# Optimization experiments

Measured on AMD Instinct MI355X. Metric: run time of the kernel, lower is better.

## Reference

```python
import jax, jax.numpy as jnp
import numpy as np

N_NODES = 50000
N_EDGES = 800000
IN_NF = 128
OUT_NF = 128
HID = 128
EDGE_NF = 16
N_LAYERS = 4
EPS = 1e-5


def _ln(x, g, b):
    mu = jnp.mean(x, axis=-1, keepdims=True)
    var = jnp.mean(jnp.square(x - mu), axis=-1, keepdims=True)
    return (x - mu) * jax.lax.rsqrt(var + EPS) * g + b


def setup_inputs() -> dict:
    key = jax.random.key(0)
    ks = iter(jax.random.split(key, 64))

    def lin(out_d, in_d):
        w = jax.random.normal(next(ks), (out_d, in_d), dtype=jnp.float32) * 0.02
        b = jnp.zeros((out_d,), dtype=jnp.float32)
        return w, b

    def stack(fn):
        outs = [fn() for _ in range(N_LAYERS)]
        return tuple(jnp.stack([o[i] for o in outs]) for i in range(len(outs[0])))

    h = jax.random.normal(next(ks), (N_NODES, IN_NF), dtype=jnp.float32)
    edges = jax.random.randint(next(ks), (2, N_EDGES), 0, N_NODES, dtype=jnp.int32)
    edge_attr = jax.random.normal(next(ks), (N_EDGES, EDGE_NF), dtype=jnp.float32)

    emb_in_w1, emb_in_b1 = lin(HID, IN_NF)
    emb_in_w2, emb_in_b2 = lin(HID, HID)
    emb_out_w1, emb_out_b1 = lin(HID, HID)
    emb_out_w2, emb_out_b2 = lin(OUT_NF, HID)

    norm_g, norm_b = stack(lambda: (jnp.ones((HID,), jnp.float32), jnp.zeros((HID,), jnp.float32)))
    edge_w1, edge_b1 = stack(lambda: lin(HID, 2 * HID + EDGE_NF))
    edge_ln_g, edge_ln_b = stack(lambda: (jnp.ones((HID,), jnp.float32), jnp.zeros((HID,), jnp.float32)))
    edge_w2, edge_b2 = stack(lambda: lin(HID, HID))
    node_w1, node_b1 = stack(lambda: lin(HID, 2 * HID))
    node_ln_g, node_ln_b = stack(lambda: (jnp.ones((HID,), jnp.float32), jnp.zeros((HID,), jnp.float32)))
    node_w2, node_b2 = stack(lambda: lin(HID, HID))

    return dict(h=h, edges=edges, edge_attr=edge_attr,
                emb_in_w1=emb_in_w1, emb_in_b1=emb_in_b1, emb_in_w2=emb_in_w2, emb_in_b2=emb_in_b2,
                norm_g=norm_g, norm_b=norm_b,
                edge_w1=edge_w1, edge_b1=edge_b1, edge_ln_g=edge_ln_g, edge_ln_b=edge_ln_b,
                edge_w2=edge_w2, edge_b2=edge_b2,
                node_w1=node_w1, node_b1=node_b1, node_ln_g=node_ln_g, node_ln_b=node_ln_b,
                node_w2=node_w2, node_b2=node_b2,
                emb_out_w1=emb_out_w1, emb_out_b1=emb_out_b1, emb_out_w2=emb_out_w2, emb_out_b2=emb_out_b2)


def _gnn(h, edges, edge_attr,
         emb_in_w1, emb_in_b1, emb_in_w2, emb_in_b2,
         norm_g, norm_b, edge_w1, edge_b1, edge_ln_g, edge_ln_b, edge_w2, edge_b2,
         node_w1, node_b1, node_ln_g, node_ln_b, node_w2, node_b2,
         emb_out_w1, emb_out_b1, emb_out_w2, emb_out_b2):
    row, col = edges[0], edges[1]
    n = h.shape[0]

    # embedding_in: Linear -> SiLU -> Linear
    h = jax.nn.silu(h @ emb_in_w1.T + emb_in_b1) @ emb_in_w2.T + emb_in_b2

    def layer(h, p):
        (ng, nb, ew1, eb1, elg, elb, ew2, eb2, nw1, nb1, nlg, nlb, nw2, nb2) = p
        hn = _ln(h, ng, nb)                                   # pre-layer LayerNorm
        # message: gather -> Linear -> LN -> SiLU -> Linear
        eh = jnp.concatenate([hn[row], hn[col], edge_attr], axis=1)  # [E, 2H+Ef]
        m = jax.nn.silu(_ln(eh @ ew1.T + eb1, elg, elb)) @ ew2.T + eb2  # [E, H]
        # aggregate: scatter-add over source nodes
        agg = jax.ops.segment_sum(m, row, num_segments=n)     # [N, H]
        cat = jnp.concatenate([hn, agg], axis=1)              # [N, 2H]
        dh = jax.nn.silu(_ln(cat @ nw1.T + nb1, nlg, nlb)) @ nw2.T + nb2
        return hn + dh, None

    params = (norm_g, norm_b, edge_w1, edge_b1, edge_ln_g, edge_ln_b, edge_w2, edge_b2,
              node_w1, node_b1, node_ln_g, node_ln_b, node_w2, node_b2)
    h, _ = jax.lax.scan(layer, h, params)

    # embedding_out
    return jax.nn.silu(h @ emb_out_w1.T + emb_out_b1) @ emb_out_w2.T + emb_out_b2


def reference(h, edges, edge_attr,
              emb_in_w1, emb_in_b1, emb_in_w2, emb_in_b2,
              norm_g, norm_b, edge_w1, edge_b1, edge_ln_g, edge_ln_b, edge_w2, edge_b2,
              node_w1, node_b1, node_ln_g, node_ln_b, node_w2, node_b2,
              emb_out_w1, emb_out_b1, emb_out_w2, emb_out_b2):
    return _gnn(h, edges, edge_attr,
                emb_in_w1, emb_in_b1, emb_in_w2, emb_in_b2,
                norm_g, norm_b, edge_w1, edge_b1, edge_ln_g, edge_ln_b, edge_w2, edge_b2,
                node_w1, node_b1, node_ln_g, node_ln_b, node_w2, node_b2,
                emb_out_w1, emb_out_b1, emb_out_w2, emb_out_b2)
```

## Files before the change

kernel.cpp:

```cpp
#include <hip/hip_runtime.h>
#include <math.h>

#define NN 50000
#define NE 800000
#define HID 128
#define NNH ((size_t)NN * HID)
#define NPAD 50176

typedef __attribute__((ext_vector_type(8))) short short8;
typedef __attribute__((ext_vector_type(4))) float f32x4;

__device__ __forceinline__ ushort f2bf(float f) {
  unsigned u = __float_as_uint(f);
  unsigned r = (u + 0x7fffu + ((u >> 16) & 1u)) >> 16;
  return (ushort)r;
}
__device__ __forceinline__ float bf2f(ushort h) {
  return __uint_as_float(((unsigned)h) << 16);
}
__device__ __forceinline__ float silu_f(float x) { return x / (1.0f + __expf(-x)); }

__global__ __launch_bounds__(256) void zero_i(int* __restrict__ p, int n)
{
  int i = blockIdx.x * 256 + threadIdx.x;
  if (i < n) p[i] = 0;
}

__global__ __launch_bounds__(256) void count_src(const int* __restrict__ src, int* __restrict__ cnt)
{
  int e = blockIdx.x * 256 + threadIdx.x;
  if (e < NE) atomicAdd(&cnt[src[e]], 1);
}

__global__ __launch_bounds__(1024) void scan_excl(const int* __restrict__ cnt, int* __restrict__ base, int n)
{
  __shared__ int ws[16];
  int t = threadIdx.x;
  const int per = (n + 1023) / 1024;
  int s0 = t * per;
  int sum = 0;
  for (int i = 0; i < per; ++i) { int idx = s0 + i; if (idx < n) sum += cnt[idx]; }
  int lane = t & 63, w = t >> 6;
  int v = sum;
  #pragma unroll
  for (int m = 1; m < 64; m <<= 1) { int o = __shfl_up(v, m, 64); if (lane >= m) v += o; }
  if (lane == 63) ws[w] = v;
  __syncthreads();
  if (t == 0) { int a = 0; for (int i = 0; i < 16; ++i) { int x = ws[i]; ws[i] = a; a += x; } }
  __syncthreads();
  int run = ws[w] + v - sum;
  for (int i = 0; i < per; ++i) {
    int idx = s0 + i;
    if (idx < n) { base[idx] = run; run += cnt[idx]; }
  }
}

__global__ __launch_bounds__(256) void place_edges(const int* __restrict__ src, const int* __restrict__ dst,
    const int* __restrict__ base, int* __restrict__ cur,
    int* __restrict__ dst_s, int* __restrict__ perm)
{
  int e = blockIdx.x * 256 + threadIdx.x;
  if (e >= NE) return;
  int s = src[e];
  int p = base[s] + atomicAdd(&cur[s], 1);
  dst_s[p] = dst[e]; perm[p] = e;
}

__global__ __launch_bounds__(256) void permute_ea_bf(const float4* __restrict__ ea,
    const int* __restrict__ perm, ushort* __restrict__ ea_s)
{
  int i = blockIdx.x * 256 + threadIdx.x;
  if (i >= NE * 4) return;
  int e = i >> 2, q = i & 3;
  float4 v = ea[(size_t)perm[e] * 4 + q];
  uint2 p;
  p.x = (uint)f2bf(v.x) | ((uint)f2bf(v.y) << 16);
  p.y = (uint)f2bf(v.z) | ((uint)f2bf(v.w) << 16);
  *(uint2*)&ea_s[(size_t)e * 16 + q * 4] = p;
}

__global__ __launch_bounds__(256) void cvt4(const float* __restrict__ s0, const float* __restrict__ s1,
    const float* __restrict__ s2, const float* __restrict__ s3, ushort* __restrict__ d)
{
  int i = blockIdx.x * 256 + threadIdx.x;
  if (i >= 65536) return;
  const float* s = (i < 16384) ? s0 : (i < 32768) ? s1 : (i < 49152) ? s2 : s3;
  d[i] = f2bf(s[i & 16383]);
}
__global__ __launch_bounds__(256) void cvt_wab(const float* __restrict__ s, ushort* __restrict__ d)
{
  int i = blockIdx.x * 256 + threadIdx.x;
  if (i >= 131072) return;
  int l = i >> 15, rem = i & 32767;
  int r = rem >> 7, c = rem & 127;
  int srow = r & 127, scol = ((r >> 7) << 7) + c;
  d[l * 104448 + r * 128 + c] = f2bf(s[(size_t)l * 34816 + srow * 272 + scol]);
}
__global__ __launch_bounds__(256) void cvt_std(const float* __restrict__ s, ushort* __restrict__ d,
    int rows, int cols, int lss)
{
  int i = blockIdx.x * 256 + threadIdx.x;
  int n = 4 * rows * cols;
  if (i >= n) return;
  int rc = rows * cols;
  int l = i / rc, rem = i - l * rc;
  d[l * 104448 + rem] = f2bf(s[(size_t)l * lss + rem]);
}

__global__ __launch_bounds__(128) void fold_w(const float* __restrict__ nw1,
    const float* __restrict__ ew2, const float* __restrict__ eb2,
    ushort* __restrict__ wu_base, float* __restrict__ nv)
{
  __shared__ float red[2];
  int bid = blockIdx.x;
  int l = bid >> 7, m = bid & 127;
  int j = threadIdx.x;
  const float* n1row = nw1 + (size_t)l * 32768 + (size_t)m * 256;
  const float* n1b = n1row + 128;
  const float* w2 = ew2 + (size_t)l * 16384;
  float s = 0.f;
  for (int k = 0; k < 128; ++k) s = fmaf(n1b[k], w2[k * 128 + j], s);
  ushort* lb = wu_base + (size_t)l * 104448;
  lb[32768 + m * 128 + j] = f2bf(s);
  lb[49152 + m * 128 + j] = f2bf(n1row[j]);
  float p = n1b[j] * eb2[l * 128 + j];
  #pragma unroll
  for (int mm = 1; mm < 64; mm <<= 1) p += __shfl_xor(p, mm, 64);
  if ((j & 63) == 0) red[j >> 6] = p;
  __syncthreads();
  if (j == 0) nv[l * 128 + m] = red[0] + red[1];
}

__global__ __launch_bounds__(256) void emb2(
    const float* __restrict__ A,
    const ushort* __restrict__ W1, const float* __restrict__ b1,
    const ushort* __restrict__ W2, const float* __restrict__ b2,
    float* __restrict__ C, int n)
{
  __shared__ ushort Al[64][136];
  const int tid = threadIdx.x;
  const int n0 = blockIdx.x * 64;

  #pragma unroll
  for (int i = 0; i < 8; ++i) {
    int s = tid + i * 256;
    int row = s >> 5, c4 = (s & 31) * 4;
    int gr = n0 + row;
    float4 v = make_float4(0.f, 0.f, 0.f, 0.f);
    if (gr < n) v = *(const float4*)(A + (size_t)gr * HID + c4);
    uint2 p;
    p.x = (uint)f2bf(v.x) | ((uint)f2bf(v.y) << 16);
    p.y = (uint)f2bf(v.z) | ((uint)f2bf(v.w) << 16);
    *(uint2*)&Al[row][c4] = p;
  }
  __syncthreads();

  const int w = tid >> 6, l = tid & 63;
  const int lr = l & 15, lh = l >> 4;

  f32x4 zf = {0.f, 0.f, 0.f, 0.f};
  f32x4 acc[8];
  #pragma unroll
  for (int nt = 0; nt < 8; ++nt) acc[nt] = zf;

  #pragma unroll
  for (int q = 0; q < 4; ++q) {
    short8 af = *(const short8*)&Al[w * 16 + lr][q * 32 + lh * 8];
    #pragma unroll
    for (int nt = 0; nt < 8; ++nt) {
      short8 bf = *(const short8*)(W1 + (size_t)(nt * 16 + lr) * HID + q * 32 + lh * 8);
      acc[nt] = __builtin_amdgcn_mfma_f32_16x16x32_bf16(af, bf, acc[nt], 0, 0, 0);
    }
  }

  float vb[8];
  #pragma unroll
  for (int nt = 0; nt < 8; ++nt) vb[nt] = b1[nt * 16 + lr];

  #pragma unroll
  for (int r = 0; r < 4; ++r) {
    int row = w * 16 + lh * 4 + r;
    #pragma unroll
    for (int nt = 0; nt < 8; ++nt)
      Al[row][nt * 16 + lr] = f2bf(silu_f(acc[nt][r] + vb[nt]));
  }

  f32x4 acc2[8];
  #pragma unroll
  for (int nt = 0; nt < 8; ++nt) acc2[nt] = zf;
  #pragma unroll
  for (int q = 0; q < 4; ++q) {
    short8 af = *(const short8*)&Al[w * 16 + lr][q * 32 + lh * 8];
    #pragma unroll
    for (int nt = 0; nt < 8; ++nt) {
      short8 bf = *(const short8*)(W2 + (size_t)(nt * 16 + lr) * HID + q * 32 + lh * 8);
      acc2[nt] = __builtin_amdgcn_mfma_f32_16x16x32_bf16(af, bf, acc2[nt], 0, 0, 0);
    }
  }

  float vb2[8];
  #pragma unroll
  for (int nt = 0; nt < 8; ++nt) vb2[nt] = b2[nt * 16 + lr];
  #pragma unroll
  for (int r = 0; r < 4; ++r) {
    int row = n0 + w * 16 + lh * 4 + r;
    if (row < n) {
      float* cr = C + (size_t)row * HID;
      #pragma unroll
      for (int nt = 0; nt < 8; ++nt)
        cr[nt * 16 + lr] = acc2[nt][r] + vb2[nt];
    }
  }
}

__global__ __launch_bounds__(256) void pab_ln(
    const float* __restrict__ Hraw, const ushort* __restrict__ Wab,
    const float* __restrict__ lg, const float* __restrict__ lbp,
    const float* __restrict__ eb1,
    float* __restrict__ Hn, float* __restrict__ Pa, float* __restrict__ Pb, int n)
{
  __shared__ float Hs[64][132];
  __shared__ ushort Al[64][136];
  const int tid = threadIdx.x;
  const int n0 = blockIdx.x * 64;

  #pragma unroll
  for (int i = 0; i < 8; ++i) {
    int s = tid + i * 256;
    int row = s >> 5, c4 = (s & 31) * 4;
    int gr = n0 + row;
    float4 v = make_float4(0.f, 0.f, 0.f, 0.f);
    if (gr < n) v = *(const float4*)(Hraw + (size_t)gr * HID + c4);
    *(float4*)&Hs[row][c4] = v;
  }
  __syncthreads();

  const int w = tid >> 6, l = tid & 63;
  const int lr = l & 15, lh = l >> 4;

  {
    const int row = w * 16 + lr;
    float s1 = 0.f, s2 = 0.f;
    #pragma unroll
    for (int j = 0; j < 8; ++j) {
      float4 v = *(float4*)&Hs[row][lh * 32 + j * 4];
      s1 += v.x + v.y + v.z + v.w;
      s2 += v.x * v.x + v.y * v.y + v.z * v.z + v.w * v.w;
    }
    s1 += __shfl_xor(s1, 16, 64); s1 += __shfl_xor(s1, 32, 64);
    s2 += __shfl_xor(s2, 16, 64); s2 += __shfl_xor(s2, 32, 64);
    float mu = s1 * (1.0f / 128.0f);
    float var = s2 * (1.0f / 128.0f) - mu * mu;
    float rs = rsqrtf(var + 1e-5f);
    int gr = n0 + row;
    #pragma unroll
    for (int j = 0; j < 8; ++j) {
      int c = lh * 32 + j * 4;
      float4 v = *(float4*)&Hs[row][c];
      float4 o;
      o.x = (v.x - mu) * rs * lg[c + 0] + lbp[c + 0];
      o.y = (v.y - mu) * rs * lg[c + 1] + lbp[c + 1];
      o.z = (v.z - mu) * rs * lg[c + 2] + lbp[c + 2];
      o.w = (v.w - mu) * rs * lg[c + 3] + lbp[c + 3];
      if (gr < n) *(float4*)(Hn + (size_t)gr * HID + c) = o;
      uint2 p;
      p.x = (uint)f2bf(o.x) | ((uint)f2bf(o.y) << 16);
      p.y = (uint)f2bf(o.z) | ((uint)f2bf(o.w) << 16);
      *(uint2*)&Al[row][c] = p;
    }
  }
  __syncthreads();

  f32x4 zf = {0.f, 0.f, 0.f, 0.f};
  f32x4 acc[16];
  #pragma unroll
  for (int nt = 0; nt < 16; ++nt) acc[nt] = zf;

  #pragma unroll
  for (int q = 0; q < 4; ++q) {
    short8 af = *(const short8*)&Al[w * 16 + lr][q * 32 + lh * 8];
    #pragma unroll
    for (int nt = 0; nt < 16; ++nt) {
      short8 bf = *(const short8*)(Wab + (size_t)(nt * 16 + lr) * HID + q * 32 + lh * 8);
      acc[nt] = __builtin_amdgcn_mfma_f32_16x16x32_bf16(af, bf, acc[nt], 0, 0, 0);
    }
  }

  float be[8];
  #pragma unroll
  for (int nt = 0; nt < 8; ++nt) be[nt] = eb1[nt * 16 + lr];

  #pragma unroll
  for (int r = 0; r < 4; ++r) {
    int row = n0 + w * 16 + lh * 4 + r;
    if (row >= n) break;
    float* pa = Pa + (size_t)row * HID;
    float* pb = Pb + (size_t)row * HID;
    #pragma unroll
    for (int nt = 0; nt < 8; ++nt) {
      int col = nt * 16 + lr;
      pa[col] = acc[nt][r] + be[nt];
      pb[col] = acc[nt + 8][r];
    }
  }
}

__global__ __launch_bounds__(256) void node_edge(
    const float* __restrict__ Pa, const float* __restrict__ Pb,
    const ushort* __restrict__ ea_bf,
    const int* __restrict__ dst_s,
    const int* __restrict__ ebase, const int* __restrict__ deg,
    const float* __restrict__ w1c,
    const float* __restrict__ elg, const float* __restrict__ elb,
    float* __restrict__ S, int n)
{
  const int tid = threadIdx.x;
  const int wv = __builtin_amdgcn_readfirstlane(tid >> 6);
  const int lane = tid & 63;
  const int node = blockIdx.x * 4 + wv;
  if (node >= n) return;
  const int c0 = lane * 2;

  float w10[16], w11[16];
  {
    const float* wr0 = w1c + (size_t)c0 * 272 + 256;
    const float* wr1 = wr0 + 272;
    #pragma unroll
    for (int q = 0; q < 4; ++q) {
      float4 a = *(const float4*)(wr0 + q * 4);
      float4 b = *(const float4*)(wr1 + q * 4);
      w10[q * 4 + 0] = a.x; w10[q * 4 + 1] = a.y; w10[q * 4 + 2] = a.z; w10[q * 4 + 3] = a.w;
      w11[q * 4 + 0] = b.x; w11[q * 4 + 1] = b.y; w11[q * 4 + 2] = b.z; w11[q * 4 + 3] = b.w;
    }
  }
  const float g0 = elg[c0], g1 = elg[c0 + 1];
  const float b0 = elb[c0], b1 = elb[c0 + 1];
  const float pax = Pa[(size_t)node * HID + c0];
  const float pay = Pa[(size_t)node * HID + c0 + 1];

  const int beg = __builtin_amdgcn_readfirstlane(ebase[node]);
  const int dg  = __builtin_amdgcn_readfirstlane(deg[node]);

  float a0 = 0.f, a1 = 0.f;

  uint4 eA0 = make_uint4(0,0,0,0), eB0 = eA0, eA1 = eA0, eB1 = eA0;
  float2 p0 = make_float2(0.f, 0.f), p1 = p0;

  auto LOADE = [&](int idx, uint4& ea, uint4& eb, float2& pb) {
    int eu = __builtin_amdgcn_readfirstlane(beg + idx);
    int d  = dst_s[eu];
    ea = *(const uint4*)(ea_bf + (size_t)eu * 16);
    eb = *(const uint4*)(ea_bf + (size_t)eu * 16 + 8);
    pb = *(const float2*)(Pb + (size_t)d * HID + c0);
  };
  auto PROCESS = [&](const uint4& eaA, const uint4& eaB, const float2& pbc) {
    float ev[16];
    uint u;
    u = eaA.x; ev[0]  = __uint_as_float(u << 16); ev[1]  = __uint_as_float(u & 0xffff0000u);
    u = eaA.y; ev[2]  = __uint_as_float(u << 16); ev[3]  = __uint_as_float(u & 0xffff0000u);
    u = eaA.z; ev[4]  = __uint_as_float(u << 16); ev[5]  = __uint_as_float(u & 0xffff0000u);
    u = eaA.w; ev[6]  = __uint_as_float(u << 16); ev[7]  = __uint_as_float(u & 0xffff0000u);
    u = eaB.x; ev[8]  = __uint_as_float(u << 16); ev[9]  = __uint_as_float(u & 0xffff0000u);
    u = eaB.y; ev[10] = __uint_as_float(u << 16); ev[11] = __uint_as_float(u & 0xffff0000u);
    u = eaB.z; ev[12] = __uint_as_float(u << 16); ev[13] = __uint_as_float(u & 0xffff0000u);
    u = eaB.w; ev[14] = __uint_as_float(u << 16); ev[15] = __uint_as_float(u & 0xffff0000u);

    float x0 = pax + pbc.x;
    float x1 = pay + pbc.y;
    #pragma unroll
    for (int k = 0; k < 16; ++k) {
      x0 = fmaf(ev[k], w10[k], x0);
      x1 = fmaf(ev[k], w11[k], x1);
    }
    float s1 = x0 + x1, s2 = x0 * x0 + x1 * x1;
    #pragma unroll
    for (int m = 1; m < 64; m <<= 1) {
      s1 += __shfl_xor(s1, m, 64);
      s2 += __shfl_xor(s2, m, 64);
    }
    float mu = s1 * (1.0f / 128.0f);
    float var = s2 * (1.0f / 128.0f) - mu * mu;
    float rs = rsqrtf(var + 1e-5f);
    a0 += silu_f((x0 - mu) * rs * g0 + b0);
    a1 += silu_f((x1 - mu) * rs * g1 + b1);
  };

  if (dg > 0) LOADE(0, eA0, eB0, p0);
  if (dg > 1) LOADE(1, eA1, eB1, p1);

  for (int i = 0; i < dg; i += 2) {
    uint4 nA0 = make_uint4(0,0,0,0), nB0 = nA0, nA1 = nA0, nB1 = nA0;
    float2 np0 = make_float2(0.f, 0.f), np1 = np0;
    if (i + 2 < dg) LOADE(i + 2, nA0, nB0, np0);
    if (i + 3 < dg) LOADE(i + 3, nA1, nB1, np1);

    PROCESS(eA0, eB0, p0);
    if (i + 1 < dg) PROCESS(eA1, eB1, p1);

    eA0 = nA0; eB0 = nB0; p0 = np0;
    eA1 = nA1; eB1 = nB1; p1 = np1;
  }

  *(float2*)(S + (size_t)node * HID + c0) = make_float2(a0, a1);
}

__global__ __launch_bounds__(256) void node_mlp(
    const float* __restrict__ Hn, const float* __restrict__ S,
    const ushort* __restrict__ N1a, const ushort* __restrict__ W2N, const ushort* __restrict__ N2,
    const float* __restrict__ nb1, const float* __restrict__ nv, const int* __restrict__ deg,
    const float* __restrict__ lng, const float* __restrict__ lnb, const float* __restrict__ nb2,
    float* __restrict__ C, int n)
{
  __shared__ ushort Ahn[64][136];
  __shared__ ushort Ah[64][136];
  __shared__ ushort Alo[64][136];
  const int tid = threadIdx.x;
  const int n0 = blockIdx.x * 64;

  #pragma unroll
  for (int i = 0; i < 8; ++i) {
    int s = tid + i * 256;
    int row = s >> 5, c4 = (s & 31) * 4;
    int gr = n0 + row;
    float4 vh = make_float4(0.f, 0.f, 0.f, 0.f);
    float4 vs = make_float4(0.f, 0.f, 0.f, 0.f);
    if (gr < n) {
      vh = *(const float4*)(Hn + (size_t)gr * HID + c4);
      vs = *(const float4*)(S + (size_t)gr * HID + c4);
    }
    uint2 ph;
    ph.x = (uint)f2bf(vh.x) | ((uint)f2bf(vh.y) << 16);
    ph.y = (uint)f2bf(vh.z) | ((uint)f2bf(vh.w) << 16);
    *(uint2*)&Ahn[row][c4] = ph;
    ushort hx = f2bf(vs.x), hy = f2bf(vs.y), hz = f2bf(vs.z), hw = f2bf(vs.w);
    uint2 ps, pl;
    ps.x = (uint)hx | ((uint)hy << 16);
    ps.y = (uint)hz | ((uint)hw << 16);
    pl.x = (uint)f2bf(vs.x - bf2f(hx)) | ((uint)f2bf(vs.y - bf2f(hy)) << 16);
    pl.y = (uint)f2bf(vs.z - bf2f(hz)) | ((uint)f2bf(vs.w - bf2f(hw)) << 16);
    *(uint2*)&Ah[row][c4]  = ps;
    *(uint2*)&Alo[row][c4] = pl;
  }
  __syncthreads();

  const int w = tid >> 6, l = tid & 63;
  const int lr = l & 15, lh = l >> 4;

  f32x4 zf = {0.f, 0.f, 0.f, 0.f};
  f32x4 acc[8];
  #pragma unroll
  for (int nt = 0; nt < 8; ++nt) acc[nt] = zf;

  #pragma unroll
  for (int q = 0; q < 4; ++q) {
    short8 an = *(const short8*)&Ahn[w * 16 + lr][q * 32 + lh * 8];
    short8 ah = *(const short8*)&Ah[w * 16 + lr][q * 32 + lh * 8];
    short8 al = *(const short8*)&Alo[w * 16 + lr][q * 32 + lh * 8];
    #pragma unroll
    for (int nt = 0; nt < 8; ++nt) {
      short8 b1f = *(const short8*)(N1a + (size_t)(nt * 16 + lr) * HID + q * 32 + lh * 8);
      short8 b2f = *(const short8*)(W2N + (size_t)(nt * 16 + lr) * HID + q * 32 + lh * 8);
      acc[nt] = __builtin_amdgcn_mfma_f32_16x16x32_bf16(an, b1f, acc[nt], 0, 0, 0);
      acc[nt] = __builtin_amdgcn_mfma_f32_16x16x32_bf16(ah, b2f, acc[nt], 0, 0, 0);
      acc[nt] = __builtin_amdgcn_mfma_f32_16x16x32_bf16(al, b2f, acc[nt], 0, 0, 0);
    }
  }

  float vb[8], vn[8], gv[8], bv[8];
  #pragma unroll
  for (int nt = 0; nt < 8; ++nt) {
    int col = nt * 16 + lr;
    vb[nt] = nb1[col]; vn[nt] = nv[col];
    gv[nt] = lng[col]; bv[nt] = lnb[col];
  }

  #pragma unroll
  for (int r = 0; r < 4; ++r) {
    int row = n0 + w * 16 + lh * 4 + r;
    float degf = (row < n) ? (float)deg[row] : 0.f;
    float vals[8];
    #pragma unroll
    for (int nt = 0; nt < 8; ++nt) vals[nt] = acc[nt][r] + vb[nt] + degf * vn[nt];
    float s1 = 0.f, s2 = 0.f;
    #pragma unroll
    for (int nt = 0; nt < 8; ++nt) { s1 += vals[nt]; s2 += vals[nt] * vals[nt]; }
    #pragma unroll
    for (int m = 1; m < 16; m <<= 1) { s1 += __shfl_xor(s1, m, 64); s2 += __shfl_xor(s2, m, 64); }
    float mu = s1 * (1.0f / 128.0f);
    float var = s2 * (1.0f / 128.0f) - mu * mu;
    float rs = rsqrtf(var + 1e-5f);
    int lrow = w * 16 + lh * 4 + r;
    #pragma unroll
    for (int nt = 0; nt < 8; ++nt)
      Ahn[lrow][nt * 16 + lr] = f2bf(silu_f((vals[nt] - mu) * rs * gv[nt] + bv[nt]));
  }

  f32x4 acc2[8];
  #pragma unroll
  for (int nt = 0; nt < 8; ++nt) acc2[nt] = zf;
  #pragma unroll
  for (int q = 0; q < 4; ++q) {
    short8 af = *(const short8*)&Ahn[w * 16 + lr][q * 32 + lh * 8];
    #pragma unroll
    for (int nt = 0; nt < 8; ++nt) {
      short8 bf = *(const short8*)(N2 + (size_t)(nt * 16 + lr) * HID + q * 32 + lh * 8);
      acc2[nt] = __builtin_amdgcn_mfma_f32_16x16x32_bf16(af, bf, acc2[nt], 0, 0, 0);
    }
  }

  float vb2[8];
  #pragma unroll
  for (int nt = 0; nt < 8; ++nt) vb2[nt] = nb2[nt * 16 + lr];
  #pragma unroll
  for (int r = 0; r < 4; ++r) {
    int row = n0 + w * 16 + lh * 4 + r;
    if (row < n) {
      const float* hr = Hn + (size_t)row * HID;
      float* cr = C + (size_t)row * HID;
      #pragma unroll
      for (int nt = 0; nt < 8; ++nt) {
        int col = nt * 16 + lr;
        cr[col] = hr[col] + acc2[nt][r] + vb2[nt];
      }
    }
  }
}

extern "C" void kernel_launch(void* const* d_in, const int* in_sizes, int n_in,
                              void* d_out, int out_size, void* d_ws, size_t ws_size,
                              hipStream_t stream)
{
  const float* in_h  = (const float*)d_in[0];
  const int*   edges = (const int*)d_in[1];
  const float* ea    = (const float*)d_in[2];
  const float* ei_w1 = (const float*)d_in[3];
  const float* ei_b1 = (const float*)d_in[4];
  const float* ei_w2 = (const float*)d_in[5];
  const float* ei_b2 = (const float*)d_in[6];
  const float* ng    = (const float*)d_in[7];
  const float* nbp   = (const float*)d_in[8];
  const float* ew1   = (const float*)d_in[9];
  const float* eb1   = (const float*)d_in[10];
  const float* elg   = (const float*)d_in[11];
  const float* elb   = (const float*)d_in[12];
  const float* ew2   = (const float*)d_in[13];
  const float* eb2   = (const float*)d_in[14];
  const float* nw1   = (const float*)d_in[15];
  const float* nb1   = (const float*)d_in[16];
  const float* nlg   = (const float*)d_in[17];
  const float* nlb   = (const float*)d_in[18];
  const float* nw2   = (const float*)d_in[19];
  const float* nb2   = (const float*)d_in[20];
  const float* eo_w1 = (const float*)d_in[21];
  const float* eo_b1 = (const float*)d_in[22];
  const float* eo_w2 = (const float*)d_in[23];
  const float* eo_b2 = (const float*)d_in[24];

  float* wf    = (float*)d_ws;
  float* B_h   = wf;
  float* B_hn  = wf + NNH;
  float* B_S   = wf + 2 * NNH;
  float* B_tmp = wf + 3 * NNH;
  float* B_pb  = wf + 4 * NNH;

  const size_t WOFF = 5 * NNH;
  ushort* wu = (ushort*)(wf + WOFF);
  const size_t SOFF = WOFF + 262144;
  int* dst_s = (int*)(wf + SOFF);
  int* cnt   = dst_s + NE;
  int* cur   = cnt + NPAD;
  int* base  = cur + NPAD;
  ushort* ea_s = (ushort*)(base + NPAD);
  float* nvb = (float*)(ea_s + (size_t)NE * 16);
  int* perm  = (int*)B_S;

  const int NB  = (NN + 63) / 64;
  const int NBE = (NN + 3) / 4;
  const int NEB = (NE + 255) / 256;

  const int* erow = edges;
  const int* ecol = edges + NE;

  zero_i<<<(2 * NPAD + 255) / 256, 256, 0, stream>>>(cnt, 2 * NPAD);
  count_src<<<NEB, 256, 0, stream>>>(erow, cnt);
  scan_excl<<<1, 1024, 0, stream>>>(cnt, base, NN);
  place_edges<<<NEB, 256, 0, stream>>>(erow, ecol, base, cur, dst_s, perm);
  permute_ea_bf<<<(NE * 4 + 255) / 256, 256, 0, stream>>>((const float4*)ea, perm, ea_s);

  cvt4<<<256, 256, 0, stream>>>(ei_w1, ei_w2, eo_w1, eo_w2, wu);
  cvt_wab<<<512, 256, 0, stream>>>(ew1, wu + 65536);
  cvt_std<<<(4 * 16384 + 255) / 256, 256, 0, stream>>>(nw2, wu + 65536 + 81920, 128, 128, 16384);
  fold_w<<<512, 128, 0, stream>>>(nw1, ew2, eb2, wu + 65536, nvb);

  emb2<<<NB, 256, 0, stream>>>(in_h, wu, ei_b1, wu + 16384, ei_b2, B_h, NN);

  for (int lyr = 0; lyr < 4; ++lyr) {
    ushort* lb = wu + 65536 + lyr * 104448;
    pab_ln<<<NB, 256, 0, stream>>>(B_h, lb, ng + 128 * lyr, nbp + 128 * lyr,
        eb1 + 128 * lyr, B_hn, B_tmp, B_pb, NN);
    node_edge<<<NBE, 256, 0, stream>>>(B_tmp, B_pb, ea_s, dst_s, base, cnt,
        ew1 + 34816 * lyr, elg + 128 * lyr, elb + 128 * lyr, B_S, NN);
    node_mlp<<<NB, 256, 0, stream>>>(B_hn, B_S, lb + 49152, lb + 32768, lb + 81920,
        nb1 + 128 * lyr, nvb + 128 * lyr, cnt,
        nlg + 128 * lyr, nlb + 128 * lyr, nb2 + 128 * lyr, B_h, NN);
  }

  emb2<<<NB, 256, 0, stream>>>(B_h, wu + 32768, eo_b1, wu + 49152, eo_b2, (float*)d_out, NN);
}
```

Before: 1.424 ms.

## Process two edges per wave with half-wave split and fp16 dot2 edge projection

Restructures the per-node edge kernel so each half-wave (32 lanes, 4 channels each) handles a different edge at once, which halves the LayerNorm shuffle-reduction depth and combines the two halves at the end. Edge attributes are now stored as fp16 instead of bf16, so the 16-wide edge-attribute projection can use packed fdot2 instructions against fp16 copies of the weights. It also adds an early exit for nodes with no edges. The costs are reduced precision in the edge-weight dot products, wasted lanes on odd-degree tails, and more live registers per lane.

```diff
diff --git a/kernel.cpp b/kernel.cpp
--- a/kernel.cpp
+++ b/kernel.cpp
@@ -9,6 +9,7 @@
 
 typedef __attribute__((ext_vector_type(8))) short short8;
 typedef __attribute__((ext_vector_type(4))) float f32x4;
+typedef __attribute__((ext_vector_type(2))) _Float16 half2v;
 
 __device__ __forceinline__ ushort f2bf(float f) {
   unsigned u = __float_as_uint(f);
@@ -17,6 +18,17 @@
 }
 __device__ __forceinline__ float bf2f(ushort h) {
   return __uint_as_float(((unsigned)h) << 16);
+}
+__device__ __forceinline__ ushort f2h_bits(float f) {
+  _Float16 h = (_Float16)f;
+  ushort u;
+  __builtin_memcpy(&u, &h, 2);
+  return u;
+}
+__device__ __forceinline__ half2v u2h(uint u) {
+  half2v h;
+  __builtin_memcpy(&h, &u, 4);
+  return h;
 }
 __device__ __forceinline__ float silu_f(float x) { return x / (1.0f + __expf(-x)); }
 
@@ -66,7 +78,7 @@
   dst_s[p] = dst[e]; perm[p] = e;
 }
 
-__global__ __launch_bounds__(256) void permute_ea_bf(const float4* __restrict__ ea,
+__global__ __launch_bounds__(256) void permute_ea_h(const float4* __restrict__ ea,
     const int* __restrict__ perm, ushort* __restrict__ ea_s)
 {
   int i = blockIdx.x * 256 + threadIdx.x;
@@ -74,8 +86,8 @@
   int e = i >> 2, q = i & 3;
   float4 v = ea[(size_t)perm[e] * 4 + q];
   uint2 p;
-  p.x = (uint)f2bf(v.x) | ((uint)f2bf(v.y) << 16);
-  p.y = (uint)f2bf(v.z) | ((uint)f2bf(v.w) << 16);
+  p.x = (uint)f2h_bits(v.x) | ((uint)f2h_bits(v.y) << 16);
+  p.y = (uint)f2h_bits(v.z) | ((uint)f2h_bits(v.w) << 16);
   *(uint2*)&ea_s[(size_t)e * 16 + q * 4] = p;
 }
 
@@ -307,7 +319,7 @@
 
 __global__ __launch_bounds__(256) void node_edge(
     const float* __restrict__ Pa, const float* __restrict__ Pb,
-    const ushort* __restrict__ ea_bf,
+    const ushort* __restrict__ ea_h,
     const int* __restrict__ dst_s,
     const int* __restrict__ ebase, const int* __restrict__ deg,
     const float* __restrict__ w1c,
@@ -319,89 +331,102 @@
   const int lane = tid & 63;
   const int node = blockIdx.x * 4 + wv;
   if (node >= n) return;
-  const int c0 = lane * 2;
-
-  float w10[16], w11[16];
-  {
-    const float* wr0 = w1c + (size_t)c0 * 272 + 256;
-    const float* wr1 = wr0 + 272;
-    #pragma unroll
-    for (int q = 0; q < 4; ++q) {
-      float4 a = *(const float4*)(wr0 + q * 4);
-      float4 b = *(const float4*)(wr1 + q * 4);
-      w10[q * 4 + 0] = a.x; w10[q * 4 + 1] = a.y; w10[q * 4 + 2] = a.z; w10[q * 4 + 3] = a.w;
-      w11[q * 4 + 0] = b.x; w11[q * 4 + 1] = b.y; w11[q * 4 + 2] = b.z; w11[q * 4 + 3] = b.w;
-    }
-  }
-  const float g0 = elg[c0], g1 = elg[c0 + 1];
-  const float b0 = elb[c0], b1 = elb[c0 + 1];
-  const float pax = Pa[(size_t)node * HID + c0];
-  const float pay = Pa[(size_t)node * HID + c0 + 1];
+  const int half = lane >> 5;
+  const int l32 = lane & 31;
+  const int c0 = l32 * 4;
 
   const int beg = __builtin_amdgcn_readfirstlane(ebase[node]);
   const int dg  = __builtin_amdgcn_readfirstlane(deg[node]);
 
-  float a0 = 0.f, a1 = 0.f;
-
-  uint4 eA0 = make_uint4(0,0,0,0), eB0 = eA0, eA1 = eA0, eB1 = eA0;
-  float2 p0 = make_float2(0.f, 0.f), p1 = p0;
-
-  auto LOADE = [&](int idx, uint4& ea, uint4& eb, float2& pb) {
-    int eu = __builtin_amdgcn_readfirstlane(beg + idx);
-    int d  = dst_s[eu];
-    ea = *(const uint4*)(ea_bf + (size_t)eu * 16);
-    eb = *(const uint4*)(ea_bf + (size_t)eu * 16 + 8);
-    pb = *(const float2*)(Pb + (size_t)d * HID + c0);
+  if (dg == 0) {
+    if (half == 0)
+      *(float4*)(S + (size_t)node * HID + c0) = make_float4(0.f, 0.f, 0.f, 0.f);
+    return;
+  }
+
+  half2v w1h[4][8];
+  #pragma unroll
+  for (int c = 0; c < 4; ++c) {
+    const float* wr = w1c + (size_t)(c0 + c) * 272 + 256;
+    #pragma unroll
+    for (int k = 0; k < 8; ++k) {
+      half2v h;
+      h[0] = (_Float16)wr[2 * k];
+      h[1] = (_Float16)wr[2 * k + 1];
+      w1h[c][k] = h;
+    }
+  }
+  const float4 gv = *(const float4*)(elg + c0);
+  const float4 bv = *(const float4*)(elb + c0);
+  const float4 pav = *(const float4*)(Pa + (size_t)node * HID + c0);
+
+  float a0 = 0.f, a1 = 0.f, a2 = 0.f, a3 = 0.f;
+
+  uint4 eC0 = make_uint4(0,0,0,0), eC1 = eC0;
+  float4 pbc = make_float4(0.f, 0.f, 0.f, 0.f);
+  bool vc = false;
+
+  auto LOADE = [&](int pairbase, uint4& e0, uint4& e1, float4& pb, bool& valid) {
+    int my = pairbase + half;
+    valid = my < dg;
+    int eu = beg + (valid ? my : dg - 1);
+    int d = dst_s[eu];
+    const ushort* ep = ea_h + (size_t)eu * 16;
+    e0 = *(const uint4*)ep;
+    e1 = *(const uint4*)(ep + 8);
+    pb = *(const float4*)(Pb + (size_t)d * HID + c0);
   };
-  auto PROCESS = [&](const uint4& eaA, const uint4& eaB, const float2& pbc) {
-    float ev[16];
-    uint u;
-    u = eaA.x; ev[0]  = __uint_as_float(u << 16); ev[1]  = __uint_as_float(u & 0xffff0000u);
-    u = eaA.y; ev[2]  = __uint_as_float(u << 16); ev[3]  = __uint_as_float(u & 0xffff0000u);
-    u = eaA.z; ev[4]  = __uint_as_float(u << 16); ev[5]  = __uint_as_float(u & 0xffff0000u);
-    u = eaA.w; ev[6]  = __uint_as_float(u << 16); ev[7]  = __uint_as_float(u & 0xffff0000u);
-    u = eaB.x; ev[8]  = __uint_as_float(u << 16); ev[9]  = __uint_as_float(u & 0xffff0000u);
-    u = eaB.y; ev[10] = __uint_as_float(u << 16); ev[11] = __uint_as_float(u & 0xffff0000u);
-    u = eaB.z; ev[12] = __uint_as_float(u << 16); ev[13] = __uint_as_float(u & 0xffff0000u);
-    u = eaB.w; ev[14] = __uint_as_float(u << 16); ev[15] = __uint_as_float(u & 0xffff0000u);
-
-    float x0 = pax + pbc.x;
-    float x1 = pay + pbc.y;
-    #pragma unroll
-    for (int k = 0; k < 16; ++k) {
-      x0 = fmaf(ev[k], w10[k], x0);
-      x1 = fmaf(ev[k], w11[k], x1);
-    }
-    float s1 = x0 + x1, s2 = x0 * x0 + x1 * x1;
-    #pragma unroll
-    for (int m = 1; m < 64; m <<= 1) {
+
+  auto PROCESS = [&](const uint4& e0, const uint4& e1, const float4& pb, bool valid) {
+    half2v eh[8];
+    eh[0] = u2h(e0.x); eh[1] = u2h(e0.y); eh[2] = u2h(e0.z); eh[3] = u2h(e0.w);
+    eh[4] = u2h(e1.x); eh[5] = u2h(e1.y); eh[6] = u2h(e1.z); eh[7] = u2h(e1.w);
+
+    float x0 = pav.x + pb.x, x1 = pav.y + pb.y, x2 = pav.z + pb.z, x3 = pav.w + pb.w;
+    #pragma unroll
+    for (int k = 0; k < 8; ++k) {
+      x0 = __builtin_amdgcn_fdot2(eh[k], w1h[0][k], x0, false);
+      x1 = __builtin_amdgcn_fdot2(eh[k], w1h[1][k], x1, false);
+      x2 = __builtin_amdgcn_fdot2(eh[k], w1h[2][k], x2, false);
+      x3 = __builtin_amdgcn_fdot2(eh[k], w1h[3][k], x3, false);
+    }
+
+    float s1 = (x0 + x1) + (x2 + x3);
+    float s2 = (x0 * x0 + x1 * x1) + (x2 * x2 + x3 * x3);
+    #pragma unroll
+    for (int m = 1; m < 32; m <<= 1) {
       s1 += __shfl_xor(s1, m, 64);
       s2 += __shfl_xor(s2, m, 64);
     }
     float mu = s1 * (1.0f / 128.0f);
     float var = s2 * (1.0f / 128.0f) - mu * mu;
     float rs = rsqrtf(var + 1e-5f);
-    a0 += silu_f((x0 - mu) * rs * g0 + b0);
-    a1 += silu_f((x1 - mu) * rs * g1 + b1);
+    float t0 = silu_f((x0 - mu) * rs * gv.x + bv.x);
+    float t1 = silu_f((x1 - mu) * rs * gv.y + bv.y);
+    float t2 = silu_f((x2 - mu) * rs * gv.z + bv.z);
+    float t3 = silu_f((x3 - mu) * rs * gv.w + bv.w);
+    if (valid) { a0 += t0; a1 += t1; a2 += t2; a3 += t3; }
   };
 
-  if (dg > 0) LOADE(0, eA0, eB0, p0);
-  if (dg > 1) LOADE(1, eA1, eB1, p1);
+  LOADE(0, eC0, eC1, pbc, vc);
 
   for (int i = 0; i < dg; i += 2) {
-    uint4 nA0 = make_uint4(0,0,0,0), nB0 = nA0, nA1 = nA0, nB1 = nA0;
-    float2 np0 = make_float2(0.f, 0.f), np1 = np0;
-    if (i + 2 < dg) LOADE(i + 2, nA0, nB0, np0);
-    if (i + 3 < dg) LOADE(i + 3, nA1, nB1, np1);
-
-    PROCESS(eA0, eB0, p0);
-    if (i + 1 < dg) PROCESS(eA1, eB1, p1);
-
-    eA0 = nA0; eB0 = nB0; p0 = np0;
-    eA1 = nA1; eB1 = nB1; p1 = np1;
-  }
-
-  *(float2*)(S + (size_t)node * HID + c0) = make_float2(a0, a1);
+    uint4 nC0 = make_uint4(0,0,0,0), nC1 = nC0;
+    float4 npb = make_float4(0.f, 0.f, 0.f, 0.f);
+    bool nv = false;
+    if (i + 2 < dg) LOADE(i + 2, nC0, nC1, npb, nv);
+
+    PROCESS(eC0, eC1, pbc, vc);
+
+    eC0 = nC0; eC1 = nC1; pbc = npb; vc = nv;
+  }
+
+  a0 += __shfl_xor(a0, 32, 64);
+  a1 += __shfl_xor(a1, 32, 64);
+  a2 += __shfl_xor(a2, 32, 64);
+  a3 += __shfl_xor(a3, 32, 64);
+  if (half == 0)
+    *(float4*)(S + (size_t)node * HID + c0) = make_float4(a0, a1, a2, a3);
 }
 
 __global__ __launch_bounds__(256) void node_mlp(
@@ -585,7 +610,7 @@
   count_src<<<NEB, 256, 0, stream>>>(erow, cnt);
   scan_excl<<<1, 1024, 0, stream>>>(cnt, base, NN);
   place_edges<<<NEB, 256, 0, stream>>>(erow, ecol, base, cur, dst_s, perm);
-  permute_ea_bf<<<(NE * 4 + 255) / 256, 256, 0, stream>>>((const float4*)ea, perm, ea_s);
+  permute_ea_h<<<(NE * 4 + 255) / 256, 256, 0, stream>>>((const float4*)ea, perm, ea_s);
 
   cvt4<<<256, 256, 0, stream>>>(ei_w1, ei_w2, eo_w1, eo_w2, wu);
   cvt_wab<<<512, 256, 0, stream>>>(ew1, wu + 65536);
```

Measured after the change: 1.663 ms. 1.17x slower.

## Fuse next-layer LayerNorm and Pa/Pb projection into emb2 and node_mlp epilogues

Applied to the files above, without the earlier changes.

The separate pab_ln kernel is removed. Its LayerNorm and the projection into the Pa/Pb edge inputs now run in the epilogues of the input-embedding kernel and of the previous layer's node_mlp, selected by a FUSE template flag. This cuts one launch per layer and avoids writing the residual H to global memory and reading it back. In exchange the epilogues use more registers, node_mlp reads and writes B_hn in place, and the LayerNorm statistics now come from cross-lane shuffles over MFMA accumulator layouts.

```diff
diff --git a/kernel.cpp b/kernel.cpp
--- a/kernel.cpp
+++ b/kernel.cpp
@@ -131,10 +131,14 @@
   if (j == 0) nv[l * 128 + m] = red[0] + red[1];
 }
 
+template<int FUSE>
 __global__ __launch_bounds__(256) void emb2(
     const float* __restrict__ A,
     const ushort* __restrict__ W1, const float* __restrict__ b1,
     const ushort* __restrict__ W2, const float* __restrict__ b2,
+    const float* __restrict__ lg, const float* __restrict__ lbp,
+    const ushort* __restrict__ Wab, const float* __restrict__ eb1,
+    float* __restrict__ Hn, float* __restrict__ Pa, float* __restrict__ Pb,
     float* __restrict__ C, int n)
 {
   __shared__ ushort Al[64][136];
@@ -201,95 +205,65 @@
   float vb2[8];
   #pragma unroll
   for (int nt = 0; nt < 8; ++nt) vb2[nt] = b2[nt * 16 + lr];
+
+  if (FUSE == 0) {
+    #pragma unroll
+    for (int r = 0; r < 4; ++r) {
+      int row = n0 + w * 16 + lh * 4 + r;
+      if (row < n) {
+        float* cr = C + (size_t)row * HID;
+        #pragma unroll
+        for (int nt = 0; nt < 8; ++nt)
+          cr[nt * 16 + lr] = acc2[nt][r] + vb2[nt];
+      }
+    }
+    return;
+  }
+
+  float gv[8], bv[8];
+  #pragma unroll
+  for (int nt = 0; nt < 8; ++nt) { gv[nt] = lg[nt * 16 + lr]; bv[nt] = lbp[nt * 16 + lr]; }
+
   #pragma unroll
   for (int r = 0; r < 4; ++r) {
     int row = n0 + w * 16 + lh * 4 + r;
-    if (row < n) {
-      float* cr = C + (size_t)row * HID;
-      #pragma unroll
-      for (int nt = 0; nt < 8; ++nt)
-        cr[nt * 16 + lr] = acc2[nt][r] + vb2[nt];
-    }
-  }
-}
-
-__global__ __launch_bounds__(256) void pab_ln(
-    const float* __restrict__ Hraw, const ushort* __restrict__ Wab,
-    const float* __restrict__ lg, const float* __restrict__ lbp,
-    const float* __restrict__ eb1,
-    float* __restrict__ Hn, float* __restrict__ Pa, float* __restrict__ Pb, int n)
-{
-  __shared__ float Hs[64][132];
-  __shared__ ushort Al[64][136];
-  const int tid = threadIdx.x;
-  const int n0 = blockIdx.x * 64;
-
-  #pragma unroll
-  for (int i = 0; i < 8; ++i) {
-    int s = tid + i * 256;
-    int row = s >> 5, c4 = (s & 31) * 4;
-    int gr = n0 + row;
-    float4 v = make_float4(0.f, 0.f, 0.f, 0.f);
-    if (gr < n) v = *(const float4*)(Hraw + (size_t)gr * HID + c4);
-    *(float4*)&Hs[row][c4] = v;
-  }
-  __syncthreads();
-
-  const int w = tid >> 6, l = tid & 63;
-  const int lr = l & 15, lh = l >> 4;
-
-  {
-    const int row = w * 16 + lr;
+    bool ok = row < n;
+    float vals[8];
+    #pragma unroll
+    for (int nt = 0; nt < 8; ++nt) vals[nt] = acc2[nt][r] + vb2[nt];
     float s1 = 0.f, s2 = 0.f;
     #pragma unroll
-    for (int j = 0; j < 8; ++j) {
-      float4 v = *(float4*)&Hs[row][lh * 32 + j * 4];
-      s1 += v.x + v.y + v.z + v.w;
-      s2 += v.x * v.x + v.y * v.y + v.z * v.z + v.w * v.w;
-    }
-    s1 += __shfl_xor(s1, 16, 64); s1 += __shfl_xor(s1, 32, 64);
-    s2 += __shfl_xor(s2, 16, 64); s2 += __shfl_xor(s2, 32, 64);
+    for (int nt = 0; nt < 8; ++nt) { s1 += vals[nt]; s2 += vals[nt] * vals[nt]; }
+    #pragma unroll
+    for (int m = 1; m < 16; m <<= 1) { s1 += __shfl_xor(s1, m, 64); s2 += __shfl_xor(s2, m, 64); }
     float mu = s1 * (1.0f / 128.0f);
     float var = s2 * (1.0f / 128.0f) - mu * mu;
     float rs = rsqrtf(var + 1e-5f);
-    int gr = n0 + row;
-    #pragma unroll
-    for (int j = 0; j < 8; ++j) {
-      int c = lh * 32 + j * 4;
-      float4 v = *(float4*)&Hs[row][c];
-      float4 o;
-      o.x = (v.x - mu) * rs * lg[c + 0] + lbp[c + 0];
-      o.y = (v.y - mu) * rs * lg[c + 1] + lbp[c + 1];
-      o.z = (v.z - mu) * rs * lg[c + 2] + lbp[c + 2];
-      o.w = (v.w - mu) * rs * lg[c + 3] + lbp[c + 3];
-      if (gr < n) *(float4*)(Hn + (size_t)gr * HID + c) = o;
-      uint2 p;
-      p.x = (uint)f2bf(o.x) | ((uint)f2bf(o.y) << 16);
-      p.y = (uint)f2bf(o.z) | ((uint)f2bf(o.w) << 16);
-      *(uint2*)&Al[row][c] = p;
-    }
-  }
-  __syncthreads();
-
-  f32x4 zf = {0.f, 0.f, 0.f, 0.f};
-  f32x4 acc[16];
-  #pragma unroll
-  for (int nt = 0; nt < 16; ++nt) acc[nt] = zf;
-
+    int lrow = w * 16 + lh * 4 + r;
+    float* hnr = Hn + (size_t)row * HID;
+    #pragma unroll
+    for (int nt = 0; nt < 8; ++nt) {
+      float hn = (vals[nt] - mu) * rs * gv[nt] + bv[nt];
+      if (ok) hnr[nt * 16 + lr] = hn;
+      Al[lrow][nt * 16 + lr] = f2bf(hn);
+    }
+  }
+
+  f32x4 aab[16];
+  #pragma unroll
+  for (int nt = 0; nt < 16; ++nt) aab[nt] = zf;
   #pragma unroll
   for (int q = 0; q < 4; ++q) {
     short8 af = *(const short8*)&Al[w * 16 + lr][q * 32 + lh * 8];
     #pragma unroll
     for (int nt = 0; nt < 16; ++nt) {
       short8 bf = *(const short8*)(Wab + (size_t)(nt * 16 + lr) * HID + q * 32 + lh * 8);
-      acc[nt] = __builtin_amdgcn_mfma_f32_16x16x32_bf16(af, bf, acc[nt], 0, 0, 0);
-    }
-  }
-
+      aab[nt] = __builtin_amdgcn_mfma_f32_16x16x32_bf16(af, bf, aab[nt], 0, 0, 0);
+    }
+  }
   float be[8];
   #pragma unroll
   for (int nt = 0; nt < 8; ++nt) be[nt] = eb1[nt * 16 + lr];
-
   #pragma unroll
   for (int r = 0; r < 4; ++r) {
     int row = n0 + w * 16 + lh * 4 + r;
@@ -299,8 +273,8 @@
     #pragma unroll
     for (int nt = 0; nt < 8; ++nt) {
       int col = nt * 16 + lr;
-      pa[col] = acc[nt][r] + be[nt];
-      pb[col] = acc[nt + 8][r];
+      pa[col] = aab[nt][r] + be[nt];
+      pb[col] = aab[nt + 8][r];
     }
   }
 }
@@ -404,11 +378,15 @@
   *(float2*)(S + (size_t)node * HID + c0) = make_float2(a0, a1);
 }
 
+template<int FUSE>
 __global__ __launch_bounds__(256) void node_mlp(
     const float* __restrict__ Hn, const float* __restrict__ S,
     const ushort* __restrict__ N1a, const ushort* __restrict__ W2N, const ushort* __restrict__ N2,
     const float* __restrict__ nb1, const float* __restrict__ nv, const int* __restrict__ deg,
     const float* __restrict__ lng, const float* __restrict__ lnb, const float* __restrict__ nb2,
+    const float* __restrict__ lg2, const float* __restrict__ lb2p,
+    const ushort* __restrict__ Wab2, const float* __restrict__ eb1_2,
+    float* __restrict__ HnOut, float* __restrict__ Pa, float* __restrict__ Pb,
     float* __restrict__ C, int n)
 {
   __shared__ ushort Ahn[64][136];
@@ -511,17 +489,84 @@
   float vb2[8];
   #pragma unroll
   for (int nt = 0; nt < 8; ++nt) vb2[nt] = nb2[nt * 16 + lr];
+
+  if (FUSE == 0) {
+    #pragma unroll
+    for (int r = 0; r < 4; ++r) {
+      int row = n0 + w * 16 + lh * 4 + r;
+      if (row < n) {
+        const float* hr = Hn + (size_t)row * HID;
+        float* cr = C + (size_t)row * HID;
+        #pragma unroll
+        for (int nt = 0; nt < 8; ++nt) {
+          int col = nt * 16 + lr;
+          cr[col] = hr[col] + acc2[nt][r] + vb2[nt];
+        }
+      }
+    }
+    return;
+  }
+
+  float gv2[8], bv2[8];
+  #pragma unroll
+  for (int nt = 0; nt < 8; ++nt) { gv2[nt] = lg2[nt * 16 + lr]; bv2[nt] = lb2p[nt * 16 + lr]; }
+
   #pragma unroll
   for (int r = 0; r < 4; ++r) {
     int row = n0 + w * 16 + lh * 4 + r;
-    if (row < n) {
-      const float* hr = Hn + (size_t)row * HID;
-      float* cr = C + (size_t)row * HID;
-      #pragma unroll
-      for (int nt = 0; nt < 8; ++nt) {
-        int col = nt * 16 + lr;
-        cr[col] = hr[col] + acc2[nt][r] + vb2[nt];
-      }
+    bool ok = row < n;
+    const float* hr = Hn + (size_t)row * HID;
+    float vals[8];
+    #pragma unroll
+    for (int nt = 0; nt < 8; ++nt) {
+      int col = nt * 16 + lr;
+      float base = ok ? hr[col] : 0.f;
+      vals[nt] = base + acc2[nt][r] + vb2[nt];
+    }
+    float s1 = 0.f, s2 = 0.f;
+    #pragma unroll
+    for (int nt = 0; nt < 8; ++nt) { s1 += vals[nt]; s2 += vals[nt] * vals[nt]; }
+    #pragma unroll
+    for (int m = 1; m < 16; m <<= 1) { s1 += __shfl_xor(s1, m, 64); s2 += __shfl_xor(s2, m, 64); }
+    float mu = s1 * (1.0f / 128.0f);
+    float var = s2 * (1.0f / 128.0f) - mu * mu;
+    float rs = rsqrtf(var + 1e-5f);
+    int lrow = w * 16 + lh * 4 + r;
+    float* hnr = HnOut + (size_t)row * HID;
+    #pragma unroll
+    for (int nt = 0; nt < 8; ++nt) {
+      float hn = (vals[nt] - mu) * rs * gv2[nt] + bv2[nt];
+      if (ok) hnr[nt * 16 + lr] = hn;
+      Ahn[lrow][nt * 16 + lr] = f2bf(hn);
+    }
+  }
+
+  f32x4 aab[16];
+  #pragma unroll
+  for (int nt = 0; nt < 16; ++nt) aab[nt] = zf;
+  #pragma unroll
+  for (int q = 0; q < 4; ++q) {
+    short8 af = *(const short8*)&Ahn[w * 16 + lr][q * 32 + lh * 8];
+    #pragma unroll
+    for (int nt = 0; nt < 16; ++nt) {
+      short8 bf = *(const short8*)(Wab2 + (size_t)(nt * 16 + lr) * HID + q * 32 + lh * 8);
+      aab[nt] = __builtin_amdgcn_mfma_f32_16x16x32_bf16(af, bf, aab[nt], 0, 0, 0);
+    }
+  }
+  float be[8];
+  #pragma unroll
+  for (int nt = 0; nt < 8; ++nt) be[nt] = eb1_2[nt * 16 + lr];
+  #pragma unroll
+  for (int r = 0; r < 4; ++r) {
+    int row = n0 + w * 16 + lh * 4 + r;
+    if (row >= n) break;
+    float* pa = Pa + (size_t)row * HID;
+    float* pb = Pb + (size_t)row * HID;
+    #pragma unroll
+    for (int nt = 0; nt < 8; ++nt) {
+      int col = nt * 16 + lr;
+      pa[col] = aab[nt][r] + be[nt];
+      pb[col] = aab[nt + 8][r];
     }
   }
 }
@@ -592,18 +637,29 @@
   cvt_std<<<(4 * 16384 + 255) / 256, 256, 0, stream>>>(nw2, wu + 65536 + 81920, 128, 128, 16384);
   fold_w<<<512, 128, 0, stream>>>(nw1, ew2, eb2, wu + 65536, nvb);
 
-  emb2<<<NB, 256, 0, stream>>>(in_h, wu, ei_b1, wu + 16384, ei_b2, B_h, NN);
+  emb2<1><<<NB, 256, 0, stream>>>(in_h, wu, ei_b1, wu + 16384, ei_b2,
+      ng, nbp, wu + 65536, eb1, B_hn, B_tmp, B_pb, nullptr, NN);
 
   for (int lyr = 0; lyr < 4; ++lyr) {
     ushort* lb = wu + 65536 + lyr * 104448;
-    pab_ln<<<NB, 256, 0, stream>>>(B_h, lb, ng + 128 * lyr, nbp + 128 * lyr,
-        eb1 + 128 * lyr, B_hn, B_tmp, B_pb, NN);
     node_edge<<<NBE, 256, 0, stream>>>(B_tmp, B_pb, ea_s, dst_s, base, cnt,
         ew1 + 34816 * lyr, elg + 128 * lyr, elb + 128 * lyr, B_S, NN);
-    node_mlp<<<NB, 256, 0, stream>>>(B_hn, B_S, lb + 49152, lb + 32768, lb + 81920,
-        nb1 + 128 * lyr, nvb + 128 * lyr, cnt,
-        nlg + 128 * lyr, nlb + 128 * lyr, nb2 + 128 * lyr, B_h, NN);
-  }
-
-  emb2<<<NB, 256, 0, stream>>>(B_h, wu + 32768, eo_b1, wu + 49152, eo_b2, (float*)d_out, NN);
-}
+    if (lyr < 3) {
+      ushort* lb2 = lb + 104448;
+      node_mlp<1><<<NB, 256, 0, stream>>>(B_hn, B_S, lb + 49152, lb + 32768, lb + 81920,
+          nb1 + 128 * lyr, nvb + 128 * lyr, cnt,
+          nlg + 128 * lyr, nlb + 128 * lyr, nb2 + 128 * lyr,
+          ng + 128 * (lyr + 1), nbp + 128 * (lyr + 1), lb2, eb1 + 128 * (lyr + 1),
+          B_hn, B_tmp, B_pb, nullptr, NN);
+    } else {
+      node_mlp<0><<<NB, 256, 0, stream>>>(B_hn, B_S, lb + 49152, lb + 32768, lb + 81920,
+          nb1 + 128 * lyr, nvb + 128 * lyr, cnt,
+          nlg + 128 * lyr, nlb + 128 * lyr, nb2 + 128 * lyr,
+          nullptr, nullptr, nullptr, nullptr,
+          nullptr, nullptr, nullptr, B_h, NN);
+    }
+  }
+
+  emb2<0><<<NB, 256, 0, stream>>>(B_h, wu + 32768, eo_b1, wu + 49152, eo_b2,
+      nullptr, nullptr, nullptr, nullptr, nullptr, nullptr, nullptr, (float*)d_out, NN);
+}
```

New measurement: 1.335 ms. -6.3%, faster.
